# Kernel optimization log

Hardware: AMD Instinct MI355X
Metric: run time of the kernel (lower is better)

## Reference

```python
import jax, jax.numpy as jnp
import numpy as np

B, T, C = 8, 2048, 1024
H, D = 16, 64
DLOW = 64  # D_DECAY = D_AAA = D_MV = D_GATE = 64
EPS_LN = 1e-5


def setup_inputs() -> dict:
    key = jax.random.key(0)
    ks = jax.random.split(key, 26)
    p = lambda k, shape, s=0.02: (jax.random.normal(k, shape, jnp.float32) * s)
    u = lambda k, shape: jax.random.uniform(k, shape, jnp.float32)
    return {
        "x":   jax.random.normal(ks[0], (B, T, C), jnp.float32),
        # token-shift mix coefficients (1,1,C)
        "x_r": u(ks[1], (1, 1, C)), "x_w": u(ks[2], (1, 1, C)),
        "x_k": u(ks[3], (1, 1, C)), "x_v": u(ks[4], (1, 1, C)),
        "x_a": u(ks[5], (1, 1, C)), "x_g": u(ks[6], (1, 1, C)),
        # decay lora: w1 [C,DLOW], w2 [DLOW,H], w0 [1,1,H,1]
        "w0": p(ks[7], (1, 1, H, 1)), "w1": p(ks[8], (C, DLOW)), "w2": p(ks[9], (DLOW, H)),
        # in-context lr lora
        "a0": p(ks[10], (1, 1, H, 1)), "a1": p(ks[11], (C, DLOW)), "a2": p(ks[12], (DLOW, H)),
        # value residual lora
        "v0": p(ks[13], (1, 1, C)), "v1": p(ks[14], (C, DLOW)), "v2": p(ks[15], (DLOW, C)),
        # gate lora
        "g1": p(ks[16], (C, DLOW)), "g2": p(ks[17], (DLOW, C)),
        "k_k": 0.85 + p(ks[18], (1, 1, C)),
        "r_k": p(ks[19], (H, D)),
        # main projections, stored [in, out] so x @ W matches nn.Linear
        "Wr": p(ks[20], (C, C)), "Wk": p(ks[21], (C, C)),
        "Wv": p(ks[22], (C, C)), "Wo": p(ks[23], (C, C)),
        # GroupNorm(n_head, n_embd) affine params
        "ln_w": jnp.ones((C,), jnp.float32) + p(ks[24], (C,)),
        "ln_b": p(ks[25], (C,)),
    }


def reference(x, x_r, x_w, x_k, x_v, x_a, x_g,
              w0, w1, w2, a0, a1, a2, v0, v1, v2, g1, g2,
              k_k, r_k, Wr, Wk, Wv, Wo, ln_w, ln_b):
    Bb, Tt, Cc = x.shape
    Hh, Dd = r_k.shape
    # token shift: sx = x_t - x_{t-1} (zero-padded)
    xx = jnp.concatenate([jnp.zeros((Bb, 1, Cc), x.dtype), x[:, :-1]], axis=1)
    sx = x - xx
    xr = x + sx * x_r
    xw = x + sx * x_w
    xk = x + sx * x_k
    xv = x + sx * x_v
    xa = x + sx * x_a
    xg = x + sx * x_g

    r = (xr @ Wr).reshape(Bb, Tt, Hh, Dd)
    # decay in (0, exp(-0.5)): exp(-softplus(-(w0 + lora)) - 0.5)
    w = jnp.exp(-jax.nn.softplus(-(w0 + (jnp.tanh(xw @ w1) @ w2).reshape(Bb, Tt, Hh, 1))) - 0.5)
    k = xk @ Wk
    v = xv @ Wv
    v_res_gate = jax.nn.sigmoid(v0 + jnp.tanh(xv @ v1) @ v2)
    v = v + (v - v) * v_res_gate  # no-op, kept for faithfulness
    a = jax.nn.sigmoid(a0 + (jnp.tanh(xa @ a1) @ a2).reshape(Bb, Tt, Hh, 1))
    g = jax.nn.sigmoid(jnp.tanh(xg @ g1) @ g2)

    kk = (k * k_k).reshape(Bb, Tt, Hh, Dd)
    kk = kk / jnp.maximum(jnp.linalg.norm(kk, axis=-1, keepdims=True), 1e-12)
    vh = v.reshape(Bb, Tt, Hh, Dd)

    # WKV linear recurrence: state = state * w_t + kk_t * v_t * a_t
    kv = (kk * vh * a).astype(jnp.float32)            # [B,T,H,D]
    w_t = jnp.moveaxis(w.astype(jnp.float32), 1, 0)   # [T,B,H,1]
    kv_t = jnp.moveaxis(kv, 1, 0)                     # [T,B,H,D]

    def step(state, inputs):
        wt, kvt = inputs
        state = state * wt + kvt
        return state, state

    init = jnp.zeros((Bb, Hh, Dd), jnp.float32)
    _, states = jax.lax.scan(step, init, (w_t, kv_t))  # [T,B,H,D]
    x_wkv = jnp.moveaxis(states, 0, 1).astype(x.dtype)  # [B,T,H,D]

    x_wkv = x_wkv * r
    bonus = jnp.sum(r * kk * r_k, axis=-1, keepdims=True) * vh
    x_wkv = x_wkv + bonus  # [B,T,H,D]

    # GroupNorm(H groups over C channels), per (B*T) sample
    mean = x_wkv.mean(axis=-1, keepdims=True)
    var = x_wkv.var(axis=-1, keepdims=True)
    xn = (x_wkv - mean) * jax.lax.rsqrt(var + EPS_LN)
    xn = xn.reshape(Bb, Tt, Cc) * ln_w + ln_b

    return (xn * g) @ Wo
```

## Files before the change

kernel.cpp:

```cpp
#include <hip/hip_runtime.h>


typedef __bf16 bf16;
typedef __attribute__((ext_vector_type(8))) __bf16 bf16x8;
typedef __attribute__((ext_vector_type(4))) float f32x4;

#define TBTOK 16384
#define TSEQ  2048
#define CDIM  1024
#define HN    16
#define CHUNK 64
#define NCH   32

__device__ __forceinline__ float wredsum(float v) {
#pragma unroll
  for (int o = 32; o > 0; o >>= 1) v += __shfl_xor(v, o, 64);
  return v;
}
__device__ __forceinline__ float qredsum(float v) {
#pragma unroll
  for (int o = 8; o > 0; o >>= 1) v += __shfl_xor(v, o, 64);
  return v;
}
__device__ __forceinline__ float sigmf(float x) { return 1.f / (1.f + expf(-x)); }

__device__ __forceinline__ void gl_lds16(const bf16* g, bf16* l) {
  __builtin_amdgcn_global_load_lds(
      (const __attribute__((address_space(1))) unsigned int*)g,
      (__attribute__((address_space(3))) unsigned int*)l, 16, 0, 0);
}

__global__ __launch_bounds__(256) void transpose_all(
    const float* __restrict__ Wr, const float* __restrict__ Wk,
    const float* __restrict__ Wv, const float* __restrict__ Wo,
    const float* __restrict__ w1, const float* __restrict__ a1, const float* __restrict__ g1,
    const float* __restrict__ mw, const float* __restrict__ ma, const float* __restrict__ mg,
    const float* __restrict__ g2, const float* __restrict__ w2, const float* __restrict__ a2,
    bf16* __restrict__ WrT, bf16* __restrict__ WkT, bf16* __restrict__ WvT, bf16* __restrict__ WoT,
    bf16* __restrict__ Bcat, bf16* __restrict__ g2T,
    bf16* __restrict__ w2T, bf16* __restrict__ a2T, float* __restrict__ zpad) {
  int bid = blockIdx.x;
  int tid = threadIdx.x;
  int tx = tid & 31, ty = tid >> 5;
  __shared__ bf16 tile[32][33];

  if (bid < 4096) {
    int sel = bid >> 10, t = bid & 1023;
    int k0 = (t >> 5) * 32, n0 = (t & 31) * 32;
    const float* src = sel == 0 ? Wr : (sel == 1 ? Wk : (sel == 2 ? Wv : Wo));
    bf16* dst = sel == 0 ? WrT : (sel == 1 ? WkT : (sel == 2 ? WvT : WoT));
#pragma unroll
    for (int i = 0; i < 4; i++)
      tile[ty + i * 8][tx] = (bf16)src[(long)(k0 + ty + i * 8) * 1024 + n0 + tx];
    __syncthreads();
#pragma unroll
    for (int i = 0; i < 4; i++)
      dst[(long)(n0 + ty + i * 8) * 1024 + k0 + tx] = tile[tx][ty + i * 8];
  } else if (bid < 4480) {
    int idx = bid - 4096;
    int mat = idx >> 7, rem = idx & 127;
    int half = rem >> 6, t = rem & 63;
    int k0 = (t >> 1) * 32, n0 = (t & 1) * 32;
    const float* W = mat == 0 ? w1 : (mat == 1 ? a1 : g1);
    const float* mx = mat == 0 ? mw : (mat == 1 ? ma : mg);
#pragma unroll
    for (int i = 0; i < 4; i++) {
      int k = k0 + ty + i * 8;
      float s = half == 0 ? (1.f + mx[k]) : (-mx[k]);
      tile[ty + i * 8][tx] = (bf16)(s * W[(long)k * 64 + n0 + tx]);
    }
    __syncthreads();
#pragma unroll
    for (int i = 0; i < 4; i++)
      Bcat[(long)(mat * 64 + n0 + ty + i * 8) * 2048 + half * 1024 + k0 + tx] =
          tile[tx][ty + i * 8];
  } else if (bid < 4544) {
    int t = bid - 4480;
    int k0 = (t >> 5) * 32, n0 = (t & 31) * 32;
#pragma unroll
    for (int i = 0; i < 4; i++)
      tile[ty + i * 8][tx] = (bf16)g2[(long)(k0 + ty + i * 8) * 1024 + n0 + tx];
    __syncthreads();
#pragma unroll
    for (int i = 0; i < 4; i++)
      g2T[(long)(n0 + ty + i * 8) * 64 + k0 + tx] = tile[tx][ty + i * 8];
  } else {
#pragma unroll
    for (int rep = 0; rep < 4; rep++) {
      int idx = rep * 256 + tid;
      int k = idx >> 4, h = idx & 15;
      w2T[h * 64 + k] = (bf16)w2[idx];
      a2T[h * 64 + k] = (bf16)a2[idx];
    }
    if (tid < 64) zpad[tid] = 0.f;
  }
}

__global__ __launch_bounds__(256) void mixcvt_kern(
    const float* __restrict__ x, const float* __restrict__ mr,
    const float* __restrict__ mk, const float* __restrict__ mv,
    bf16* __restrict__ xr, bf16* __restrict__ xk, bf16* __restrict__ xv,
    bf16* __restrict__ xbf) {
  long i8 = ((long)blockIdx.x * 256 + threadIdx.x) * 8;
  int m = (int)(i8 >> 10);
  int c = (int)(i8 & 1023);
  f32x4 x0 = *(const f32x4*)(x + i8);
  f32x4 x1 = *(const f32x4*)(x + i8 + 4);
  f32x4 p0 = {0.f, 0.f, 0.f, 0.f}, p1 = {0.f, 0.f, 0.f, 0.f};
  if ((m & (TSEQ - 1)) != 0) {
    p0 = *(const f32x4*)(x + i8 - CDIM);
    p1 = *(const f32x4*)(x + i8 - CDIM + 4);
  }
  f32x4 r0 = *(const f32x4*)(mr + c), r1 = *(const f32x4*)(mr + c + 4);
  f32x4 k0 = *(const f32x4*)(mk + c), k1 = *(const f32x4*)(mk + c + 4);
  f32x4 v0 = *(const f32x4*)(mv + c), v1 = *(const f32x4*)(mv + c + 4);
  bf16x8 or_, ok_, ov_, ox_;
#pragma unroll
  for (int j = 0; j < 4; j++) {
    float s0 = x0[j] - p0[j], s1 = x1[j] - p1[j];
    or_[j] = (bf16)(x0[j] + s0 * r0[j]); or_[4 + j] = (bf16)(x1[j] + s1 * r1[j]);
    ok_[j] = (bf16)(x0[j] + s0 * k0[j]); ok_[4 + j] = (bf16)(x1[j] + s1 * k1[j]);
    ov_[j] = (bf16)(x0[j] + s0 * v0[j]); ov_[4 + j] = (bf16)(x1[j] + s1 * v1[j]);
    ox_[j] = (bf16)x0[j];                ox_[4 + j] = (bf16)x1[j];
  }
  *(bf16x8*)(xr + i8) = or_;
  *(bf16x8*)(xk + i8) = ok_;
  *(bf16x8*)(xv + i8) = ov_;
  *(bf16x8*)(xbf + i8) = ox_;
}

template <int ACT, typename OT>
__global__ __launch_bounds__(256) void gemm128_kern(
    const bf16* __restrict__ A0, const bf16* __restrict__ A1, const bf16* __restrict__ A2,
    int apitch, int acol0,
    const bf16* __restrict__ BT0, const bf16* __restrict__ BT1, const bf16* __restrict__ BT2,
    OT* __restrict__ out0, OT* __restrict__ out1, OT* __restrict__ out2,
    int opitch, int K, int nbpm) {
  int by = blockIdx.y;
  int mat = by / nbpm;
  int ncol0 = (by % nbpm) * 128;
  const bf16* Am = mat == 0 ? A0 : (mat == 1 ? A1 : A2);
  const bf16* BTm = mat == 0 ? BT0 : (mat == 1 ? BT1 : BT2);
  OT* out = mat == 0 ? out0 : (mat == 1 ? out1 : out2);
  int m0 = blockIdx.x * 128;

  __shared__ bf16 Al[128 * 32];
  __shared__ bf16 Bl[128 * 32];

  int tid = threadIdx.x;
  int w = tid >> 6, lane = tid & 63, quad = lane >> 4, lr = lane & 15;
  int wm = (w & 1) * 64, wn = (w >> 1) * 64;

  f32x4 acc[4][4] = {};

  int r0 = tid >> 2, kc0 = (tid & 3) * 8;
  const bf16* ag0 = Am + (long)(m0 + r0) * apitch + acol0 + kc0;
  const bf16* ag1 = ag0 + (long)64 * apitch;
  const bf16* bg0 = BTm + (long)(ncol0 + r0) * K + kc0;
  const bf16* bg1 = bg0 + (long)64 * K;
  bf16* la0 = Al + w * 512;
  bf16* la1 = Al + 2048 + w * 512;
  bf16* lb0 = Bl + w * 512;
  bf16* lb1 = Bl + 2048 + w * 512;

  for (int k0 = 0; k0 < K; k0 += 32) {
    gl_lds16(ag0, la0);
    gl_lds16(ag1, la1);
    gl_lds16(bg0, lb0);
    gl_lds16(bg1, lb1);
    ag0 += 32; ag1 += 32; bg0 += 32; bg1 += 32;
    __syncthreads();
    bf16x8 af[4], bff[4];
#pragma unroll
    for (int i = 0; i < 4; i++) af[i] = *(const bf16x8*)&Al[(wm + i * 16 + lr) * 32 + quad * 8];
#pragma unroll
    for (int j = 0; j < 4; j++) bff[j] = *(const bf16x8*)&Bl[(wn + j * 16 + lr) * 32 + quad * 8];
#pragma unroll
    for (int i = 0; i < 4; i++)
#pragma unroll
      for (int j = 0; j < 4; j++)
        acc[i][j] = __builtin_amdgcn_mfma_f32_16x16x32_bf16(af[i], bff[j], acc[i][j], 0, 0, 0);
    __syncthreads();
  }
#pragma unroll
  for (int i = 0; i < 4; i++)
#pragma unroll
    for (int j = 0; j < 4; j++)
#pragma unroll
      for (int rg = 0; rg < 4; rg++) {
        int row = m0 + wm + i * 16 + quad * 4 + rg;
        int col = ncol0 + wn + j * 16 + lr;
        float v = acc[i][j][rg];
        if (ACT == 1) v = sigmf(v);
        out[(long)row * opitch + col] = (OT)v;
      }
}

__global__ __launch_bounds__(256) void stage1_diag(
    const bf16* __restrict__ xbf, const bf16* __restrict__ Bcat,
    const float* __restrict__ zpad, bf16* __restrict__ t1) {
  int m0 = blockIdx.x * 64;
  __shared__ bf16 Al[64 * 32];
  __shared__ bf16 Bl[192 * 32];

  int tid = threadIdx.x;
  int w = tid >> 6, lane = tid & 63, quad = lane >> 4, lr = lane & 15;
  int wm = w * 16;

  f32x4 acc[12] = {};

  int r0 = tid >> 2, kc0 = (tid & 3) * 8;
  int m = m0 + r0;
  const bf16* asrc = xbf + (long)m * CDIM + kc0;
  bool firstrow = (m & (TSEQ - 1)) == 0;
  const bf16* psrc = firstrow ? (const bf16*)zpad : xbf + (long)(m - 1) * CDIM + kc0;
  int pstep = firstrow ? 0 : 32;
  const bf16* bs0 = Bcat + (long)(r0)       * 2048 + kc0;
  const bf16* bs1 = Bcat + (long)(r0 + 64)  * 2048 + kc0;
  const bf16* bs2 = Bcat + (long)(r0 + 128) * 2048 + kc0;
  bf16* la = Al + w * 512;
  bf16* lb0 = Bl + w * 512;
  bf16* lb1 = Bl + 2048 + w * 512;
  bf16* lb2 = Bl + 4096 + w * 512;

#pragma unroll 1
  for (int kk = 0; kk < 64; kk++) {
    if (kk < 32) {
      gl_lds16(asrc, la);
      asrc += 32;
    } else {
      gl_lds16(psrc, la);
      psrc += pstep;
    }
    gl_lds16(bs0, lb0);
    gl_lds16(bs1, lb1);
    gl_lds16(bs2, lb2);
    bs0 += 32; bs1 += 32; bs2 += 32;
    __syncthreads();
    bf16x8 af = *(const bf16x8*)&Al[(wm + lr) * 32 + quad * 8];
#pragma unroll
    for (int nf = 0; nf < 12; nf++) {
      bf16x8 bff = *(const bf16x8*)&Bl[(nf * 16 + lr) * 32 + quad * 8];
      acc[nf] = __builtin_amdgcn_mfma_f32_16x16x32_bf16(af, bff, acc[nf], 0, 0, 0);
    }
    __syncthreads();
  }
#pragma unroll
  for (int nf = 0; nf < 12; nf++)
#pragma unroll
    for (int rg = 0; rg < 4; rg++) {
      int row = m0 + wm + quad * 4 + rg;
      int col = nf * 16 + lr;
      t1[(long)row * 192 + col] = (bf16)tanhf(acc[nf][rg]);
    }
}

__global__ __launch_bounds__(256) void stage2_wa(
    const bf16* __restrict__ t1, const bf16* __restrict__ w2T, const bf16* __restrict__ a2T,
    const float* __restrict__ w0, const float* __restrict__ a0,
    float* __restrict__ w_arr, float* __restrict__ a_arr) {
  int tid = blockIdx.x * 256 + threadIdx.x;
  int m = tid >> 4, h = tid & 15;
  float dw = 0.f, da = 0.f;
  const bf16* rw = t1 + (long)m * 192;
  const bf16* ra = rw + 64;
  const bf16* ww = w2T + h * 64;
  const bf16* aw = a2T + h * 64;
#pragma unroll
  for (int k8 = 0; k8 < 8; k8++) {
    bf16x8 tw = *(const bf16x8*)(rw + k8 * 8);
    bf16x8 ta = *(const bf16x8*)(ra + k8 * 8);
    bf16x8 cw = *(const bf16x8*)(ww + k8 * 8);
    bf16x8 ca = *(const bf16x8*)(aw + k8 * 8);
#pragma unroll
    for (int j = 0; j < 8; j++) {
      dw += (float)tw[j] * (float)cw[j];
      da += (float)ta[j] * (float)ca[j];
    }
  }
  w_arr[h * TBTOK + m] = 0.60653066f * sigmf(w0[h] + dw);
  a_arr[h * TBTOK + m] = sigmf(a0[h] + da);
}

__global__ __launch_bounds__(256) void scan1_kern(
    const bf16* __restrict__ k_buf, const bf16* __restrict__ v_buf, const bf16* __restrict__ r_buf,
    const float* __restrict__ k_k, const float* __restrict__ r_k,
    const float* __restrict__ a_arr, const float* __restrict__ w_arr,
    float* __restrict__ kv2, float* __restrict__ Parr, float* __restrict__ bonus) {
  int wid = blockIdx.x * 4 + (threadIdx.x >> 6);
  int lane = threadIdx.x & 63;
  int bh = wid >> 5, c = wid & 31;
  int b = bh >> 4, h = bh & 15;
  int mstart = b * TSEQ + c * CHUNK;
  int kc = h * 64 + lane;
  float kkc = k_k[kc], rkc = r_k[kc];
  float st = 0.f, cw = 1.f;
  long mbase = (long)mstart * CDIM + kc;
  int hm = h * TBTOK + mstart;
  long sbase = ((long)hm) * 64 + lane;
  float kf = (float)k_buf[mbase] * kkc;
  float vf = (float)v_buf[mbase];
  float rf = (float)r_buf[mbase];
  float af = a_arr[hm];
  float wt = w_arr[hm];
  for (int t = 0; t < CHUNK; t++) {
    float kf_n = 0.f, vf_n = 0.f, rf_n = 0.f, af_n = 0.f, wt_n = 0.f;
    if (t < CHUNK - 1) {
      kf_n = (float)k_buf[mbase + CDIM] * kkc;
      vf_n = (float)v_buf[mbase + CDIM];
      rf_n = (float)r_buf[mbase + CDIM];
      af_n = a_arr[hm + 1];
      wt_n = w_arr[hm + 1];
    }
    float ss = wredsum(kf * kf);
    float kkn = kf / fmaxf(sqrtf(ss), 1e-12f);
    st = st * wt + kkn * vf * af;
    kv2[sbase] = st;
    cw *= wt;
    float bs = wredsum(rf * kkn * rkc);
    if (lane == 0) {
      Parr[hm] = cw;
      bonus[(mstart + t) * HN + h] = bs;
    }
    kf = kf_n; vf = vf_n; rf = rf_n; af = af_n; wt = wt_n;
    mbase += CDIM; hm += 1; sbase += 64;
  }
}

__global__ __launch_bounds__(64) void scan2_kern(const float* __restrict__ kv2,
                                                 const float* __restrict__ Parr,
                                                 float* __restrict__ carry) {
  int bh = blockIdx.x;
  int h = bh >> 3, b = bh & 7;
  int lane = threadIdx.x;
  float S = 0.f;
  for (int c = 0; c < NCH; c++) {
    carry[(((h * 8 + b) * NCH) + c) * 64 + lane] = S;
    int mlast = b * TSEQ + c * CHUNK + (CHUNK - 1);
    float L = kv2[((long)(h * TBTOK + mlast)) * 64 + lane];
    float pw = Parr[h * TBTOK + mlast];
    S = L + pw * S;
  }
}

__global__ __launch_bounds__(256) void gate_post_kern(
    const bf16* __restrict__ t1, const bf16* __restrict__ g2T,
    const float* __restrict__ kv2, const float* __restrict__ Parr,
    const float* __restrict__ carry, const float* __restrict__ bonus,
    bf16* __restrict__ r_buf, const bf16* __restrict__ v_buf,
    const float* __restrict__ ln_w, const float* __restrict__ ln_b) {
  int ncol0 = blockIdx.y * 128;
  int m0 = blockIdx.x * 128;

  __shared__ bf16 Al[128 * 32];
  __shared__ bf16 Bl[128 * 32];

  int tid = threadIdx.x;
  int w = tid >> 6, lane = tid & 63, quad = lane >> 4, lr = lane & 15;
  int wm = (w & 1) * 64, wn = (w >> 1) * 64;

  f32x4 acc[4][4] = {};

  int r0 = tid >> 2, kc0 = (tid & 3) * 8;
  const bf16* ag0 = t1 + (long)(m0 + r0) * 192 + 128 + kc0;
  const bf16* ag1 = ag0 + (long)64 * 192;
  const bf16* bg0 = g2T + (long)(ncol0 + r0) * 64 + kc0;
  const bf16* bg1 = bg0 + (long)64 * 64;
  bf16* la0 = Al + w * 512;
  bf16* la1 = Al + 2048 + w * 512;
  bf16* lb0 = Bl + w * 512;
  bf16* lb1 = Bl + 2048 + w * 512;

  for (int k0 = 0; k0 < 64; k0 += 32) {
    gl_lds16(ag0, la0);
    gl_lds16(ag1, la1);
    gl_lds16(bg0, lb0);
    gl_lds16(bg1, lb1);
    ag0 += 32; ag1 += 32; bg0 += 32; bg1 += 32;
    __syncthreads();
    bf16x8 af[4], bff[4];
#pragma unroll
    for (int i = 0; i < 4; i++) af[i] = *(const bf16x8*)&Al[(wm + i * 16 + lr) * 32 + quad * 8];
#pragma unroll
    for (int j = 0; j < 4; j++) bff[j] = *(const bf16x8*)&Bl[(wn + j * 16 + lr) * 32 + quad * 8];
#pragma unroll
    for (int i = 0; i < 4; i++)
#pragma unroll
      for (int j = 0; j < 4; j++)
        acc[i][j] = __builtin_amdgcn_mfma_f32_16x16x32_bf16(af[i], bff[j], acc[i][j], 0, 0, 0);
    __syncthreads();
  }

  int col0 = ncol0 + wn;
  int h = col0 >> 6;
  int b = m0 >> 11;
  int ch = ((m0 + wm) & (TSEQ - 1)) >> 6;
  float cy[4], lnwv[4], lnbv[4];
#pragma unroll
  for (int j = 0; j < 4; j++) {
    int d = j * 16 + lr;
    cy[j] = carry[((h * 8 + b) * NCH + ch) * 64 + d];
    lnwv[j] = ln_w[col0 + d];
    lnbv[j] = ln_b[col0 + d];
  }
#pragma unroll
  for (int i = 0; i < 4; i++)
#pragma unroll
    for (int rg = 0; rg < 4; rg++) {
      int row = m0 + wm + i * 16 + quad * 4 + rg;
      float pw = Parr[h * TBTOK + row];
      float bs = bonus[row * HN + h];
      long kvb = ((long)h * TBTOK + row) * 64;
      long rb = (long)row * CDIM + col0;
      float xw[4];
#pragma unroll
      for (int j = 0; j < 4; j++) {
        int d = j * 16 + lr;
        float st = kv2[kvb + d] + pw * cy[j];
        float rf = (float)r_buf[rb + d];
        float vf = (float)v_buf[rb + d];
        xw[j] = st * rf + bs * vf;
      }
      float sum = xw[0] + xw[1] + xw[2] + xw[3];
      float mn = qredsum(sum) * (1.f / 64.f);
      float vs = 0.f;
#pragma unroll
      for (int j = 0; j < 4; j++) {
        xw[j] -= mn;
        vs += xw[j] * xw[j];
      }
      float var = qredsum(vs) * (1.f / 64.f);
      float rq = rsqrtf(var + 1e-5f);
#pragma unroll
      for (int j = 0; j < 4; j++) {
        int d = j * 16 + lr;
        float y = xw[j] * rq * lnwv[j] + lnbv[j];
        float gv = sigmf(acc[i][j][rg]);
        r_buf[rb + d] = (bf16)(y * gv);
      }
    }
}

extern "C" void kernel_launch(void* const* d_in, const int* in_sizes, int n_in,
                              void* d_out, int out_size, void* d_ws, size_t ws_size,
                              hipStream_t stream) {
  const float* x    = (const float*)d_in[0];
  const float* x_r  = (const float*)d_in[1];
  const float* x_w  = (const float*)d_in[2];
  const float* x_k  = (const float*)d_in[3];
  const float* x_v  = (const float*)d_in[4];
  const float* x_a  = (const float*)d_in[5];
  const float* x_g  = (const float*)d_in[6];
  const float* w0   = (const float*)d_in[7];
  const float* w1   = (const float*)d_in[8];
  const float* w2   = (const float*)d_in[9];
  const float* a0   = (const float*)d_in[10];
  const float* a1   = (const float*)d_in[11];
  const float* a2   = (const float*)d_in[12];
  const float* g1   = (const float*)d_in[16];
  const float* g2   = (const float*)d_in[17];
  const float* k_k  = (const float*)d_in[18];
  const float* r_k  = (const float*)d_in[19];
  const float* Wr   = (const float*)d_in[20];
  const float* Wk   = (const float*)d_in[21];
  const float* Wv   = (const float*)d_in[22];
  const float* Wo   = (const float*)d_in[23];
  const float* ln_w = (const float*)d_in[24];
  const float* ln_b = (const float*)d_in[25];
  float* out = (float*)d_out;

  char* p = (char*)d_ws;
  auto carve = [&](size_t bytes) {
    void* r = (void*)p;
    p += (bytes + 255) & ~(size_t)255;
    return r;
  };
  bf16* WrT = (bf16*)carve(1024 * 1024 * 2);
  bf16* WkT = (bf16*)carve(1024 * 1024 * 2);
  bf16* WvT = (bf16*)carve(1024 * 1024 * 2);
  bf16* WoT = (bf16*)carve(1024 * 1024 * 2);
  bf16* Bcat = (bf16*)carve(192 * 2048 * 2);
  bf16* g2T  = (bf16*)carve(1024 * 64 * 2);
  bf16* w2T  = (bf16*)carve(16 * 64 * 2);
  bf16* a2T  = (bf16*)carve(16 * 64 * 2);
  float* zpad = (float*)carve(64 * 4);
  bf16* t1    = (bf16*)carve((size_t)TBTOK * 192 * 2);
  bf16* r_buf = (bf16*)carve((size_t)TBTOK * CDIM * 2);
  bf16* k_buf = (bf16*)carve((size_t)TBTOK * CDIM * 2);
  bf16* v_buf = (bf16*)carve((size_t)TBTOK * CDIM * 2);
  float* w_arr = (float*)carve((size_t)TBTOK * HN * 4);
  float* a_arr = (float*)carve((size_t)TBTOK * HN * 4);
  float* bonus = (float*)carve((size_t)TBTOK * HN * 4);
  float* Parr  = (float*)carve((size_t)TBTOK * HN * 4);
  float* carry = (float*)carve((size_t)128 * NCH * 64 * 4);
  bf16* xr  = (bf16*)carve((size_t)TBTOK * CDIM * 2);
  bf16* xk  = (bf16*)carve((size_t)TBTOK * CDIM * 2);
  bf16* xv  = (bf16*)carve((size_t)TBTOK * CDIM * 2);
  bf16* xbf = (bf16*)carve((size_t)TBTOK * CDIM * 2);
  float* kv2 = (float*)xv;

  transpose_all<<<dim3(4545), 256, 0, stream>>>(
      Wr, Wk, Wv, Wo, w1, a1, g1, x_w, x_a, x_g, g2, w2, a2,
      WrT, WkT, WvT, WoT, Bcat, g2T, w2T, a2T, zpad);
  mixcvt_kern<<<dim3(TBTOK * CDIM / 2048), 256, 0, stream>>>(
      x, x_r, x_k, x_v, xr, xk, xv, xbf);
  stage1_diag<<<dim3(TBTOK / 64), 256, 0, stream>>>(xbf, Bcat, zpad, t1);
  stage2_wa<<<dim3(TBTOK * HN / 256), 256, 0, stream>>>(t1, w2T, a2T, w0, a0, w_arr, a_arr);
  gemm128_kern<0, bf16><<<dim3(TBTOK / 128, 24), 256, 0, stream>>>(
      xr, xk, xv, CDIM, 0, WrT, WkT, WvT,
      r_buf, k_buf, v_buf, CDIM, 1024, 8);
  scan1_kern<<<dim3(128 * NCH / 4), 256, 0, stream>>>(
      k_buf, v_buf, r_buf, k_k, r_k, a_arr, w_arr, kv2, Parr, bonus);
  scan2_kern<<<dim3(128), 64, 0, stream>>>(kv2, Parr, carry);
  gate_post_kern<<<dim3(TBTOK / 128, 8), 256, 0, stream>>>(
      t1, g2T, kv2, Parr, carry, bonus, r_buf, v_buf, ln_w, ln_b);
  gemm128_kern<0, float><<<dim3(TBTOK / 128, 8), 256, 0, stream>>>(
      r_buf, r_buf, r_buf, CDIM, 0, WoT, WoT, WoT,
      out, out, out, CDIM, 1024, 8);
}
```

Measured before the change: 592.0 us.

## Fuse prep kernels, fold decay/lr projection into stage1, widen GEMM K-tile with swizzle

Merges the token-shift mix/convert kernel into the weight-transpose kernel so one launch covers both. Folds the small w/a LoRA second projections into stage1 via an LDS tile, which removes the stage2 launch and shrinks the t1 buffer to only the gate slice. The main GEMM now loads a 64-wide K tile per sync with an XOR-swizzled LDS layout, halving barriers and aiming to avoid bank conflicts, at the cost of doubled LDS per block. The stage1 epilogue now does a scalar 64-term dot per thread, which may add latency there.

```diff
diff --git a/kernel.cpp b/kernel.cpp
--- a/kernel.cpp
+++ b/kernel.cpp
@@ -30,7 +30,11 @@
       (__attribute__((address_space(3))) unsigned int*)l, 16, 0, 0);
 }
 
-__global__ __launch_bounds__(256) void transpose_all(
+__global__ __launch_bounds__(256) void prep_kern(
+    const float* __restrict__ x, const float* __restrict__ mr,
+    const float* __restrict__ mk, const float* __restrict__ mv,
+    bf16* __restrict__ xr, bf16* __restrict__ xk, bf16* __restrict__ xv,
+    bf16* __restrict__ xbf,
     const float* __restrict__ Wr, const float* __restrict__ Wk,
     const float* __restrict__ Wv, const float* __restrict__ Wo,
     const float* __restrict__ w1, const float* __restrict__ a1, const float* __restrict__ g1,
@@ -39,11 +43,40 @@
     bf16* __restrict__ WrT, bf16* __restrict__ WkT, bf16* __restrict__ WvT, bf16* __restrict__ WoT,
     bf16* __restrict__ Bcat, bf16* __restrict__ g2T,
     bf16* __restrict__ w2T, bf16* __restrict__ a2T, float* __restrict__ zpad) {
-  int bid = blockIdx.x;
+  int bid0 = blockIdx.x;
   int tid = threadIdx.x;
+  if (bid0 < 8192) {
+    long i8 = ((long)bid0 * 256 + tid) * 8;
+    int m = (int)(i8 >> 10);
+    int c = (int)(i8 & 1023);
+    f32x4 x0 = *(const f32x4*)(x + i8);
+    f32x4 x1 = *(const f32x4*)(x + i8 + 4);
+    f32x4 p0 = {0.f, 0.f, 0.f, 0.f}, p1 = {0.f, 0.f, 0.f, 0.f};
+    if ((m & (TSEQ - 1)) != 0) {
+      p0 = *(const f32x4*)(x + i8 - CDIM);
+      p1 = *(const f32x4*)(x + i8 - CDIM + 4);
+    }
+    f32x4 r0 = *(const f32x4*)(mr + c), r1 = *(const f32x4*)(mr + c + 4);
+    f32x4 k0 = *(const f32x4*)(mk + c), k1 = *(const f32x4*)(mk + c + 4);
+    f32x4 v0 = *(const f32x4*)(mv + c), v1 = *(const f32x4*)(mv + c + 4);
+    bf16x8 or_, ok_, ov_, ox_;
+#pragma unroll
+    for (int j = 0; j < 4; j++) {
+      float s0 = x0[j] - p0[j], s1 = x1[j] - p1[j];
+      or_[j] = (bf16)(x0[j] + s0 * r0[j]); or_[4 + j] = (bf16)(x1[j] + s1 * r1[j]);
+      ok_[j] = (bf16)(x0[j] + s0 * k0[j]); ok_[4 + j] = (bf16)(x1[j] + s1 * k1[j]);
+      ov_[j] = (bf16)(x0[j] + s0 * v0[j]); ov_[4 + j] = (bf16)(x1[j] + s1 * v1[j]);
+      ox_[j] = (bf16)x0[j];                ox_[4 + j] = (bf16)x1[j];
+    }
+    *(bf16x8*)(xr + i8) = or_;
+    *(bf16x8*)(xk + i8) = ok_;
+    *(bf16x8*)(xv + i8) = ov_;
+    *(bf16x8*)(xbf + i8) = ox_;
+    return;
+  }
+  int bid = bid0 - 8192;
   int tx = tid & 31, ty = tid >> 5;
   __shared__ bf16 tile[32][33];
-
   if (bid < 4096) {
     int sel = bid >> 10, t = bid & 1023;
     int k0 = (t >> 5) * 32, n0 = (t & 31) * 32;
@@ -96,43 +129,10 @@
   }
 }
 
-__global__ __launch_bounds__(256) void mixcvt_kern(
-    const float* __restrict__ x, const float* __restrict__ mr,
-    const float* __restrict__ mk, const float* __restrict__ mv,
-    bf16* __restrict__ xr, bf16* __restrict__ xk, bf16* __restrict__ xv,
-    bf16* __restrict__ xbf) {
-  long i8 = ((long)blockIdx.x * 256 + threadIdx.x) * 8;
-  int m = (int)(i8 >> 10);
-  int c = (int)(i8 & 1023);
-  f32x4 x0 = *(const f32x4*)(x + i8);
-  f32x4 x1 = *(const f32x4*)(x + i8 + 4);
-  f32x4 p0 = {0.f, 0.f, 0.f, 0.f}, p1 = {0.f, 0.f, 0.f, 0.f};
-  if ((m & (TSEQ - 1)) != 0) {
-    p0 = *(const f32x4*)(x + i8 - CDIM);
-    p1 = *(const f32x4*)(x + i8 - CDIM + 4);
-  }
-  f32x4 r0 = *(const f32x4*)(mr + c), r1 = *(const f32x4*)(mr + c + 4);
-  f32x4 k0 = *(const f32x4*)(mk + c), k1 = *(const f32x4*)(mk + c + 4);
-  f32x4 v0 = *(const f32x4*)(mv + c), v1 = *(const f32x4*)(mv + c + 4);
-  bf16x8 or_, ok_, ov_, ox_;
-#pragma unroll
-  for (int j = 0; j < 4; j++) {
-    float s0 = x0[j] - p0[j], s1 = x1[j] - p1[j];
-    or_[j] = (bf16)(x0[j] + s0 * r0[j]); or_[4 + j] = (bf16)(x1[j] + s1 * r1[j]);
-    ok_[j] = (bf16)(x0[j] + s0 * k0[j]); ok_[4 + j] = (bf16)(x1[j] + s1 * k1[j]);
-    ov_[j] = (bf16)(x0[j] + s0 * v0[j]); ov_[4 + j] = (bf16)(x1[j] + s1 * v1[j]);
-    ox_[j] = (bf16)x0[j];                ox_[4 + j] = (bf16)x1[j];
-  }
-  *(bf16x8*)(xr + i8) = or_;
-  *(bf16x8*)(xk + i8) = ok_;
-  *(bf16x8*)(xv + i8) = ov_;
-  *(bf16x8*)(xbf + i8) = ox_;
-}
-
 template <int ACT, typename OT>
 __global__ __launch_bounds__(256) void gemm128_kern(
     const bf16* __restrict__ A0, const bf16* __restrict__ A1, const bf16* __restrict__ A2,
-    int apitch, int acol0,
+    int apitch,
     const bf16* __restrict__ BT0, const bf16* __restrict__ BT1, const bf16* __restrict__ BT2,
     OT* __restrict__ out0, OT* __restrict__ out1, OT* __restrict__ out2,
     int opitch, int K, int nbpm) {
@@ -144,8 +144,8 @@
   OT* out = mat == 0 ? out0 : (mat == 1 ? out1 : out2);
   int m0 = blockIdx.x * 128;
 
-  __shared__ bf16 Al[128 * 32];
-  __shared__ bf16 Bl[128 * 32];
+  __shared__ bf16 Al[128 * 64];
+  __shared__ bf16 Bl[128 * 64];
 
   int tid = threadIdx.x;
   int w = tid >> 6, lane = tid & 63, quad = lane >> 4, lr = lane & 15;
@@ -153,33 +153,42 @@
 
   f32x4 acc[4][4] = {};
 
-  int r0 = tid >> 2, kc0 = (tid & 3) * 8;
-  const bf16* ag0 = Am + (long)(m0 + r0) * apitch + acol0 + kc0;
-  const bf16* ag1 = ag0 + (long)64 * apitch;
-  const bf16* bg0 = BTm + (long)(ncol0 + r0) * K + kc0;
-  const bf16* bg1 = bg0 + (long)64 * K;
-  bf16* la0 = Al + w * 512;
-  bf16* la1 = Al + 2048 + w * 512;
-  bf16* lb0 = Bl + w * 512;
-  bf16* lb1 = Bl + 2048 + w * 512;
-
-  for (int k0 = 0; k0 < K; k0 += 32) {
-    gl_lds16(ag0, la0);
-    gl_lds16(ag1, la1);
-    gl_lds16(bg0, lb0);
-    gl_lds16(bg1, lb1);
-    ag0 += 32; ag1 += 32; bg0 += 32; bg1 += 32;
-    __syncthreads();
-    bf16x8 af[4], bff[4];
-#pragma unroll
-    for (int i = 0; i < 4; i++) af[i] = *(const bf16x8*)&Al[(wm + i * 16 + lr) * 32 + quad * 8];
-#pragma unroll
-    for (int j = 0; j < 4; j++) bff[j] = *(const bf16x8*)&Bl[(wn + j * 16 + lr) * 32 + quad * 8];
-#pragma unroll
-    for (int i = 0; i < 4; i++)
-#pragma unroll
-      for (int j = 0; j < 4; j++)
-        acc[i][j] = __builtin_amdgcn_mfma_f32_16x16x32_bf16(af[i], bff[j], acc[i][j], 0, 0, 0);
+  int r0 = tid >> 3;
+  int slot = tid & 7;
+  int kg = (slot ^ (r0 & 7)) * 8;
+  const bf16* ag = Am + (long)(m0 + r0) * apitch + kg;
+  const bf16* bg = BTm + (long)(ncol0 + r0) * K + kg;
+  long astep = (long)32 * apitch;
+  long bstep = (long)32 * K;
+  bf16* la = Al + w * 512;
+  bf16* lb = Bl + w * 512;
+
+  for (int k0 = 0; k0 < K; k0 += 64) {
+#pragma unroll
+    for (int s = 0; s < 4; s++) gl_lds16(ag + s * astep, la + s * 2048);
+#pragma unroll
+    for (int s = 0; s < 4; s++) gl_lds16(bg + s * bstep, lb + s * 2048);
+    ag += 64; bg += 64;
+    __syncthreads();
+#pragma unroll
+    for (int ko = 0; ko < 2; ko++) {
+      bf16x8 af[4], bff[4];
+#pragma unroll
+      for (int i = 0; i < 4; i++) {
+        int ra = wm + i * 16 + lr;
+        af[i] = *(const bf16x8*)&Al[ra * 64 + (((ko * 4 + quad) ^ (ra & 7)) * 8)];
+      }
+#pragma unroll
+      for (int j = 0; j < 4; j++) {
+        int rb = wn + j * 16 + lr;
+        bff[j] = *(const bf16x8*)&Bl[rb * 64 + (((ko * 4 + quad) ^ (rb & 7)) * 8)];
+      }
+#pragma unroll
+      for (int i = 0; i < 4; i++)
+#pragma unroll
+        for (int j = 0; j < 4; j++)
+          acc[i][j] = __builtin_amdgcn_mfma_f32_16x16x32_bf16(af[i], bff[j], acc[i][j], 0, 0, 0);
+    }
     __syncthreads();
   }
 #pragma unroll
@@ -196,12 +205,15 @@
       }
 }
 
-__global__ __launch_bounds__(256) void stage1_diag(
+__global__ __launch_bounds__(256) void stage1_kern(
     const bf16* __restrict__ xbf, const bf16* __restrict__ Bcat,
-    const float* __restrict__ zpad, bf16* __restrict__ t1) {
+    const float* __restrict__ zpad, const bf16* __restrict__ w2T, const bf16* __restrict__ a2T,
+    const float* __restrict__ w0, const float* __restrict__ a0,
+    bf16* __restrict__ t1g, float* __restrict__ w_arr, float* __restrict__ a_arr) {
   int m0 = blockIdx.x * 64;
   __shared__ bf16 Al[64 * 32];
   __shared__ bf16 Bl[192 * 32];
+  __shared__ bf16 Lt1[64 * 128];
 
   int tid = threadIdx.x;
   int w = tid >> 6, lane = tid & 63, quad = lane >> 4, lr = lane & 15;
@@ -249,37 +261,29 @@
   for (int nf = 0; nf < 12; nf++)
 #pragma unroll
     for (int rg = 0; rg < 4; rg++) {
-      int row = m0 + wm + quad * 4 + rg;
-      int col = nf * 16 + lr;
-      t1[(long)row * 192 + col] = (bf16)tanhf(acc[nf][rg]);
-    }
-}
-
-__global__ __launch_bounds__(256) void stage2_wa(
-    const bf16* __restrict__ t1, const bf16* __restrict__ w2T, const bf16* __restrict__ a2T,
-    const float* __restrict__ w0, const float* __restrict__ a0,
-    float* __restrict__ w_arr, float* __restrict__ a_arr) {
-  int tid = blockIdx.x * 256 + threadIdx.x;
-  int m = tid >> 4, h = tid & 15;
-  float dw = 0.f, da = 0.f;
-  const bf16* rw = t1 + (long)m * 192;
-  const bf16* ra = rw + 64;
-  const bf16* ww = w2T + h * 64;
-  const bf16* aw = a2T + h * 64;
-#pragma unroll
-  for (int k8 = 0; k8 < 8; k8++) {
-    bf16x8 tw = *(const bf16x8*)(rw + k8 * 8);
-    bf16x8 ta = *(const bf16x8*)(ra + k8 * 8);
-    bf16x8 cw = *(const bf16x8*)(ww + k8 * 8);
-    bf16x8 ca = *(const bf16x8*)(aw + k8 * 8);
-#pragma unroll
-    for (int j = 0; j < 8; j++) {
-      dw += (float)tw[j] * (float)cw[j];
-      da += (float)ta[j] * (float)ca[j];
-    }
-  }
-  w_arr[h * TBTOK + m] = 0.60653066f * sigmf(w0[h] + dw);
-  a_arr[h * TBTOK + m] = sigmf(a0[h] + da);
+      int row = wm + quad * 4 + rg;
+      float tv = tanhf(acc[nf][rg]);
+      if (nf < 8) Lt1[row * 128 + nf * 16 + lr] = (bf16)tv;
+      else t1g[(long)(m0 + row) * 64 + (nf - 8) * 16 + lr] = (bf16)tv;
+    }
+  __syncthreads();
+#pragma unroll
+  for (int rep = 0; rep < 4; rep++) {
+    int idx = rep * 256 + tid;
+    int row = idx >> 4, h = idx & 15;
+    const bf16* rw = &Lt1[row * 128];
+    const bf16* ra = rw + 64;
+    const bf16* ww = w2T + h * 64;
+    const bf16* aw = a2T + h * 64;
+    float dw = 0.f, da = 0.f;
+#pragma unroll
+    for (int k = 0; k < 64; k++) {
+      dw += (float)rw[k] * (float)ww[k];
+      da += (float)ra[k] * (float)aw[k];
+    }
+    w_arr[h * TBTOK + m0 + row] = 0.60653066f * sigmf(w0[h] + dw);
+    a_arr[h * TBTOK + m0 + row] = sigmf(a0[h] + da);
+  }
 }
 
 __global__ __launch_bounds__(256) void scan1_kern(
@@ -344,7 +348,7 @@
 }
 
 __global__ __launch_bounds__(256) void gate_post_kern(
-    const bf16* __restrict__ t1, const bf16* __restrict__ g2T,
+    const bf16* __restrict__ t1g, const bf16* __restrict__ g2T,
     const float* __restrict__ kv2, const float* __restrict__ Parr,
     const float* __restrict__ carry, const float* __restrict__ bonus,
     bf16* __restrict__ r_buf, const bf16* __restrict__ v_buf,
@@ -362,8 +366,8 @@
   f32x4 acc[4][4] = {};
 
   int r0 = tid >> 2, kc0 = (tid & 3) * 8;
-  const bf16* ag0 = t1 + (long)(m0 + r0) * 192 + 128 + kc0;
-  const bf16* ag1 = ag0 + (long)64 * 192;
+  const bf16* ag0 = t1g + (long)(m0 + r0) * 64 + kc0;
+  const bf16* ag1 = ag0 + (long)64 * 64;
   const bf16* bg0 = g2T + (long)(ncol0 + r0) * 64 + kc0;
   const bf16* bg1 = bg0 + (long)64 * 64;
   bf16* la0 = Al + w * 512;
@@ -484,7 +488,7 @@
   bf16* w2T  = (bf16*)carve(16 * 64 * 2);
   bf16* a2T  = (bf16*)carve(16 * 64 * 2);
   float* zpad = (float*)carve(64 * 4);
-  bf16* t1    = (bf16*)carve((size_t)TBTOK * 192 * 2);
+  bf16* t1g   = (bf16*)carve((size_t)TBTOK * 64 * 2);
   bf16* r_buf = (bf16*)carve((size_t)TBTOK * CDIM * 2);
   bf16* k_buf = (bf16*)carve((size_t)TBTOK * CDIM * 2);
   bf16* v_buf = (bf16*)carve((size_t)TBTOK * CDIM * 2);
@@ -499,22 +503,21 @@
   bf16* xbf = (bf16*)carve((size_t)TBTOK * CDIM * 2);
   float* kv2 = (float*)xv;
 
-  transpose_all<<<dim3(4545), 256, 0, stream>>>(
+  prep_kern<<<dim3(8192 + 4545), 256, 0, stream>>>(
+      x, x_r, x_k, x_v, xr, xk, xv, xbf,
       Wr, Wk, Wv, Wo, w1, a1, g1, x_w, x_a, x_g, g2, w2, a2,
       WrT, WkT, WvT, WoT, Bcat, g2T, w2T, a2T, zpad);
-  mixcvt_kern<<<dim3(TBTOK * CDIM / 2048), 256, 0, stream>>>(
-      x, x_r, x_k, x_v, xr, xk, xv, xbf);
-  stage1_diag<<<dim3(TBTOK / 64), 256, 0, stream>>>(xbf, Bcat, zpad, t1);
-  stage2_wa<<<dim3(TBTOK * HN / 256), 256, 0, stream>>>(t1, w2T, a2T, w0, a0, w_arr, a_arr);
+  stage1_kern<<<dim3(TBTOK / 64), 256, 0, stream>>>(
+      xbf, Bcat, zpad, w2T, a2T, w0, a0, t1g, w_arr, a_arr);
   gemm128_kern<0, bf16><<<dim3(TBTOK / 128, 24), 256, 0, stream>>>(
-      xr, xk, xv, CDIM, 0, WrT, WkT, WvT,
+      xr, xk, xv, CDIM, WrT, WkT, WvT,
       r_buf, k_buf, v_buf, CDIM, 1024, 8);
   scan1_kern<<<dim3(128 * NCH / 4), 256, 0, stream>>>(
       k_buf, v_buf, r_buf, k_k, r_k, a_arr, w_arr, kv2, Parr, bonus);
   scan2_kern<<<dim3(128), 64, 0, stream>>>(kv2, Parr, carry);
   gate_post_kern<<<dim3(TBTOK / 128, 8), 256, 0, stream>>>(
-      t1, g2T, kv2, Parr, carry, bonus, r_buf, v_buf, ln_w, ln_b);
+      t1g, g2T, kv2, Parr, carry, bonus, r_buf, v_buf, ln_w, ln_b);
   gemm128_kern<0, float><<<dim3(TBTOK / 128, 8), 256, 0, stream>>>(
-      r_buf, r_buf, r_buf, CDIM, 0, WoT, WoT, WoT,
+      r_buf, r_buf, r_buf, CDIM, WoT, WoT, WoT,
       out, out, out, CDIM, 1024, 8);
 }
```

Result: no change. 583.9 us (-1.4%).
